# Kernel optimization log

Measured on AMD Instinct MI355X. Metric: run time of the kernel, lower is better.

## Reference

```python
import jax, jax.numpy as jnp
import numpy as np

N, C, V, L = 32, 32, 400, 64
GH_IN, GH = 64, [128, 64]
NUM_GRAPHS, ORDER, K, ALPHA = 2, 2, 20, 0.05
OUT_CH = 32
CAT_CH = C * (NUM_GRAPHS * ORDER + 1)
BN_EPS = 1e-5


def setup_inputs() -> dict:
    key = jax.random.key(0)
    ks = jax.random.split(key, 12)
    s = lambda fan_in: 1.0 / np.sqrt(fan_in)
    return {
        "inputs": jax.random.normal(ks[0], (N, C, V, L), jnp.float32),
        "adj_mats": jax.random.normal(ks[1], (V, V, GH_IN), jnp.float32),
        # edge MLP: Linear(64->128), ReLU, Linear(128->64), ReLU, Linear(64->num_graphs)
        "mlp_w0": jax.random.normal(ks[2], (GH_IN, GH[0]), jnp.float32) * s(GH_IN),
        "mlp_b0": jnp.zeros((GH[0],), jnp.float32),
        "mlp_w1": jax.random.normal(ks[3], (GH[0], GH[1]), jnp.float32) * s(GH[0]),
        "mlp_b1": jnp.zeros((GH[1],), jnp.float32),
        "mlp_w2": jax.random.normal(ks[4], (GH[1], NUM_GRAPHS), jnp.float32) * s(GH[1]),
        "mlp_b2": jnp.zeros((NUM_GRAPHS,), jnp.float32),
        # 1x1 Conv2d(in=160, out=32) == channel-mixing matmul
        "conv_w": jax.random.normal(ks[5], (OUT_CH, CAT_CH), jnp.float32) * s(CAT_CH),
        "conv_b": jnp.zeros((OUT_CH,), jnp.float32),
        "bn_gamma": jnp.ones((OUT_CH,), jnp.float32),
        "bn_beta": jnp.zeros((OUT_CH,), jnp.float32),
    }


def _sparsify(logits):
    # logits: [V, V]; softmax over rows, keep top-K per row, renormalize.
    adj = jax.nn.softmax(logits, axis=1)
    _, idx = jax.lax.top_k(adj, K)                     # [V, K]
    mask = jnp.zeros((V, V), adj.dtype).at[jnp.arange(V)[:, None], idx].set(1.0)
    adj = adj * mask
    return adj / (adj.sum(axis=1, keepdims=True) + 1e-8)


def reference(inputs, adj_mats, mlp_w0, mlp_b0, mlp_w1, mlp_b1, mlp_w2, mlp_b2,
              conv_w, conv_b, bn_gamma, bn_beta):
    # edge MLP on [V, V, GH_IN] -> [V, V, NUM_GRAPHS]
    h = jax.nn.relu(adj_mats @ mlp_w0 + mlp_b0)
    h = jax.nn.relu(h @ mlp_w1 + mlp_b1)
    g = h @ mlp_w2 + mlp_b2
    A = jax.vmap(_sparsify)(jnp.moveaxis(g, 2, 0))     # [NUM_GRAPHS, V, V]

    x = jax.nn.relu(inputs)                            # [N, C, V, L]
    outs = [x]
    for i in range(NUM_GRAPHS):
        y = x
        for _ in range(ORDER):
            y = ALPHA * x + (1.0 - ALPHA) * jnp.einsum('ncvl,vw->ncwl', y, A[i])
            outs.append(y)
    x1 = jnp.concatenate(outs, axis=1)                 # [N, CAT_CH, V, L]
    out = jnp.einsum('ncvl,oc->novl', x1, conv_w) + conv_b[None, :, None, None]

    # BatchNorm2d, training mode (batch statistics, biased variance)
    mean = out.mean(axis=(0, 2, 3), keepdims=True)
    var = out.var(axis=(0, 2, 3), keepdims=True)
    out = (out - mean) * jax.lax.rsqrt(var + BN_EPS)
    out = out * bn_gamma[None, :, None, None] + bn_beta[None, :, None, None]
    return out
```

## Files before the change

### kernel.cpp

```cpp
#include <hip/hip_runtime.h>


#define VDIM 400
#define VP   416
#define KV   (4*VP)
#define EROWS (5*VP)
#define OL   2048
#define ALPHA_ 0.05f
#define BETA_  0.95f

typedef short  bf16x8 __attribute__((ext_vector_type(8)));
typedef float  f32x4  __attribute__((ext_vector_type(4)));

__device__ inline unsigned short f2bf(float x){
  unsigned int u = __float_as_uint(x);
  unsigned int r = (u + 0x7fffu + ((u >> 16) & 1u)) >> 16;
  return (unsigned short)r;
}
__device__ inline float bf2f(unsigned short u){
  return __uint_as_float(((unsigned int)u) << 16);
}

__global__ __launch_bounds__(256) void k_mlp3(
    const float* __restrict__ adj,
    const float* __restrict__ w0, const float* __restrict__ b0,
    const float* __restrict__ w1, const float* __restrict__ b1,
    const float* __restrict__ w2, const float* __restrict__ b2,
    float* __restrict__ g)
{
  __shared__ __align__(16) float s_inT[64*68];
  __shared__ __align__(16) float s_h1 [64*72];
  __shared__ __align__(16) float s_red[4*64*2];
  const int tid  = threadIdx.x;
  const long ebase = (long)blockIdx.x * 64;
  const int wid  = __builtin_amdgcn_readfirstlane(tid >> 6);
  const int lane = tid & 63;

  #pragma unroll
  for (int i = 0; i < 4; ++i){
    const int idx = tid + i*256;
    const int row = idx >> 4, f4 = (idx & 15)*4;
    f32x4 v = *reinterpret_cast<const f32x4*>(&adj[(ebase + row)*64 + f4]);
    s_inT[(f4+0)*68 + row] = v.x;
    s_inT[(f4+1)*68 + row] = v.y;
    s_inT[(f4+2)*68 + row] = v.z;
    s_inT[(f4+3)*68 + row] = v.w;
  }
  __syncthreads();

  const int n0 = wid * 32;
  float h0[32];
  #pragma unroll
  for (int j = 0; j < 32; ++j) h0[j] = b0[n0 + j];
  #pragma unroll 2
  for (int f = 0; f < 64; ++f){
    const float a = s_inT[f*68 + lane];
    const float* __restrict__ wr = &w0[f*128 + n0];
    #pragma unroll
    for (int j = 0; j < 32; ++j) h0[j] = fmaf(a, wr[j], h0[j]);
  }
  #pragma unroll
  for (int j = 0; j < 32; ++j) h0[j] = fmaxf(h0[j], 0.f);

  float p[64];
  #pragma unroll
  for (int nh = 0; nh < 2; ++nh){
    float acc1[32];
    #pragma unroll
    for (int j = 0; j < 32; ++j) acc1[j] = 0.f;
    #pragma unroll 2
    for (int f = 0; f < 32; ++f){
      const float hv = h0[f];
      const float* __restrict__ wr = &w1[(n0 + f)*64 + nh*32];
      #pragma unroll
      for (int j = 0; j < 32; ++j) acc1[j] = fmaf(hv, wr[j], acc1[j]);
    }
    #pragma unroll
    for (int j = 0; j < 32; ++j) p[nh*32 + j] = acc1[j];
  }

  #pragma unroll
  for (int w = 0; w < 4; ++w){
    if (wid == w){
      if (w == 0){
        #pragma unroll
        for (int j = 0; j < 64; j += 4){
          f32x4 v = { p[j] + b1[j],   p[j+1] + b1[j+1],
                      p[j+2] + b1[j+2], p[j+3] + b1[j+3] };
          *reinterpret_cast<f32x4*>(&s_h1[lane*72 + j]) = v;
        }
      } else {
        #pragma unroll
        for (int j = 0; j < 64; j += 4){
          f32x4 v = *reinterpret_cast<f32x4*>(&s_h1[lane*72 + j]);
          v.x += p[j]; v.y += p[j+1]; v.z += p[j+2]; v.w += p[j+3];
          *reinterpret_cast<f32x4*>(&s_h1[lane*72 + j]) = v;
        }
      }
    }
    __syncthreads();
  }

  float q0 = 0.f, q1 = 0.f;
  #pragma unroll
  for (int j = 0; j < 16; ++j){
    const int n = wid*16 + j;
    const float hv = fmaxf(s_h1[lane*72 + n], 0.f);
    q0 = fmaf(hv, w2[n*2 + 0], q0);
    q1 = fmaf(hv, w2[n*2 + 1], q1);
  }
  s_red[(wid*64 + lane)*2 + 0] = q0;
  s_red[(wid*64 + lane)*2 + 1] = q1;
  __syncthreads();
  if (wid == 0){
    float r0 = b2[0], r1 = b2[1];
    #pragma unroll
    for (int w = 0; w < 4; ++w){
      r0 += s_red[(w*64 + lane)*2 + 0];
      r1 += s_red[(w*64 + lane)*2 + 1];
    }
    g[(ebase + lane)*2 + 0] = r0;
    g[(ebase + lane)*2 + 1] = r1;
  }
}

__global__ __launch_bounds__(256) void k_sparsify(
    const float* __restrict__ g, float* __restrict__ Bf)
{
  const int row = blockIdx.x, gr = blockIdx.y, tid = threadIdx.x;
  const int wid = tid >> 6, lane = tid & 63;
  __shared__ float s_v[4]; __shared__ int s_i[4];
  __shared__ float s_p[512];
  __shared__ int   s_sel[512];
  const int i0 = tid, i1 = tid + 256;
  float v0 = (i0 < VDIM) ? g[(row*VDIM + i0)*2 + gr] : -3.4e38f;
  float v1 = (i1 < VDIM) ? g[(row*VDIM + i1)*2 + gr] : -3.4e38f;

  float m = fmaxf(v0, v1);
  for (int off = 32; off > 0; off >>= 1) m = fmaxf(m, __shfl_down(m, off, 64));
  if (lane == 0) s_v[wid] = m;
  __syncthreads();
  const float rowmax = fmaxf(fmaxf(s_v[0], s_v[1]), fmaxf(s_v[2], s_v[3]));
  float p0 = (i0 < VDIM) ? expf(v0 - rowmax) : 0.f;
  float p1 = (i1 < VDIM) ? expf(v1 - rowmax) : 0.f;
  float zs = p0 + p1;
  for (int off = 32; off > 0; off >>= 1) zs += __shfl_down(zs, off, 64);
  __syncthreads();
  if (lane == 0) s_v[wid] = zs;
  __syncthreads();
  const float Z = s_v[0] + s_v[1] + s_v[2] + s_v[3];
  p0 /= Z; p1 /= Z;
  s_p[i0] = p0; s_p[i1] = p1;
  s_sel[i0] = (i0 < VDIM) ? 0 : 1;
  s_sel[i1] = (i1 < VDIM) ? 0 : 1;
  __syncthreads();

  float ssum = 0.f;
  for (int it = 0; it < 20; ++it){
    float cv = -1.f; int ci = 0x7fffffff;
    if (!s_sel[i0])              { cv = p0; ci = i0; }
    if (!s_sel[i1] && (p1 > cv)) { cv = p1; ci = i1; }
    for (int off = 32; off > 0; off >>= 1){
      float ov = __shfl_down(cv, off, 64); int oi = __shfl_down(ci, off, 64);
      if (ov > cv || (ov == cv && oi < ci)){ cv = ov; ci = oi; }
    }
    if (lane == 0){ s_v[wid] = cv; s_i[wid] = ci; }
    __syncthreads();
    float wv = s_v[0]; int wi_ = s_i[0];
    #pragma unroll
    for (int k = 1; k < 4; ++k){
      float ov = s_v[k]; int oi = s_i[k];
      if (ov > wv || (ov == wv && oi < wi_)){ wv = ov; wi_ = oi; }
    }
    ssum += wv;
    if (tid == (wi_ & 255)) s_sel[wi_] = 1;
    __syncthreads();
  }
  const float inv = 1.0f / (ssum + 1e-8f);
  float* B1 = Bf + (size_t)(gr*2) * (VDIM*VDIM);
  if (i0 < VDIM) B1[(size_t)i0*VDIM + row] = s_sel[i0] ? (s_p[i0]*inv) : 0.f;
  if (i1 < VDIM) B1[(size_t)i1*VDIM + row] = s_sel[i1] ? (s_p[i1]*inv) : 0.f;
}

__global__ __launch_bounds__(256) void k_sq(float* __restrict__ Bf)
{
  const int gr = blockIdx.z;
  const float* S = Bf + (size_t)(2*gr)   * (VDIM*VDIM);
  float*       D = Bf + (size_t)(2*gr+1) * (VDIM*VDIM);
  const int tx = threadIdx.x & 15, ty = threadIdx.x >> 4;
  const int w = blockIdx.x*16 + ty, v = blockIdx.y*16 + tx;
  __shared__ float As[16][17], Bs[16][17];
  float acc = 0.f;
  for (int u0 = 0; u0 < VDIM; u0 += 16){
    As[ty][tx] = S[(size_t)w*VDIM + u0 + tx];
    Bs[ty][tx] = S[(size_t)(u0+ty)*VDIM + v];
    __syncthreads();
    #pragma unroll
    for (int u = 0; u < 16; ++u) acc += As[ty][u] * Bs[u][tx];
    __syncthreads();
  }
  D[(size_t)w*VDIM + v] = acc;
}

__global__ __launch_bounds__(256) void k_pack(
    const float* __restrict__ Bf, const float* __restrict__ conv_w,
    unsigned short* __restrict__ Bcat, unsigned short* __restrict__ Mpp,
    float* __restrict__ bns)
{
  const int idx = blockIdx.x*256 + threadIdx.x;
  if (idx < 512*KV){
    const int w = idx / KV, col = idx % KV;
    const int k1 = col / VP, v = col % VP;
    float val = (w < VDIM && v < VDIM) ? Bf[(size_t)k1*(VDIM*VDIM) + (size_t)w*VDIM + v] : 0.f;
    Bcat[idx] = f2bf(val);
  }
  if (blockIdx.x == 0){
    const float a = ALPHA_, b = BETA_;
    for (int mIdx = threadIdx.x; mIdx < 160*32; mIdx += 256){
      const int rowm = mIdx >> 5, c = mIdx & 31;
      const int k = rowm / 32, o = rowm & 31;
      float W[5];
      #pragma unroll
      for (int j = 0; j < 5; ++j) W[j] = conv_w[o*160 + j*32 + c];
      float val;
      if      (k == 0) val = W[0] + a*(W[1]+W[2]+W[3]+W[4]);
      else if (k == 1) val = b*W[1] + a*b*W[2];
      else if (k == 2) val = b*b*W[2];
      else if (k == 3) val = b*W[3] + a*b*W[4];
      else             val = b*b*W[4];
      Mpp[rowm*32 + c] = f2bf(val);
    }
    if (threadIdx.x < 64) bns[threadIdx.x] = 0.f;
  }
}

__global__ __launch_bounds__(640) void k_e(
    const float* __restrict__ x, const unsigned short* __restrict__ Mpp,
    unsigned short* __restrict__ e, int n0)
{
  const int v0 = blockIdx.x * 2;
  const int n = n0 + blockIdx.y;
  const int tid = threadIdx.x;
  unsigned short* en = e + (size_t)blockIdx.y * EROWS * OL;
  if (v0 >= VDIM){
    for (int i = tid; i < 5*256*2; i += 640){
      const int row = i >> 8;
      const int k = row >> 1, vv = row & 1;
      const int off = (i & 255) * 8;
      *reinterpret_cast<uint4*>(&en[(size_t)(k*VP + v0 + vv)*OL + off]) = make_uint4(0,0,0,0);
    }
    return;
  }
  __shared__ __align__(16) unsigned short s_xT[64*32];
  __shared__ __align__(16) unsigned short s_out[10*16*64];
  const int wid = tid >> 6, lane = tid & 63;
  const int l15 = lane & 15, q = lane >> 4;
  bf16x8 afrag = *reinterpret_cast<const bf16x8*>(&Mpp[(wid*16 + l15)*32 + q*8]);
  const f32x4 zero = {0.f, 0.f, 0.f, 0.f};

  #pragma unroll
  for (int vv = 0; vv < 2; ++vv){
    const int v = v0 + vv;
    if (vv) __syncthreads();
    if (tid < 512){
      const int c = tid >> 4, l4 = (tid & 15) * 4;
      float4 xv = *reinterpret_cast<const float4*>(x + ((size_t)n*32 + c)*25600 + (size_t)v*64 + l4);
      s_xT[(l4+0)*32 + c] = f2bf(fmaxf(xv.x, 0.f));
      s_xT[(l4+1)*32 + c] = f2bf(fmaxf(xv.y, 0.f));
      s_xT[(l4+2)*32 + c] = f2bf(fmaxf(xv.z, 0.f));
      s_xT[(l4+3)*32 + c] = f2bf(fmaxf(xv.w, 0.f));
    }
    __syncthreads();
    f32x4 acc[4];
    #pragma unroll
    for (int lt = 0; lt < 4; ++lt){
      bf16x8 bfrag = *reinterpret_cast<const bf16x8*>(&s_xT[(lt*16 + l15)*32 + q*8]);
      acc[lt] = __builtin_amdgcn_mfma_f32_16x16x32_bf16(afrag, bfrag, zero, 0, 0, 0);
    }
    unsigned short* so = &s_out[wid*1024];
    #pragma unroll
    for (int lt = 0; lt < 4; ++lt)
      #pragma unroll
      for (int r = 0; r < 4; ++r)
        so[(q*4 + r)*64 + lt*16 + l15] = f2bf(acc[lt][r]);
    const int k = wid >> 1, o0 = (wid & 1) * 16;
    const size_t gbase = (size_t)(k*VP + v)*OL + (size_t)o0*64;
    uint4 d0 = *reinterpret_cast<uint4*>(&so[lane*16]);
    uint4 d1 = *reinterpret_cast<uint4*>(&so[lane*16 + 8]);
    *reinterpret_cast<uint4*>(&en[gbase + lane*16])     = d0;
    *reinterpret_cast<uint4*>(&en[gbase + lane*16 + 8]) = d1;
  }
}

__global__ __launch_bounds__(256) void k_prop(
    const unsigned short* __restrict__ Bcat, const unsigned short* __restrict__ e,
    const float* __restrict__ conv_b, float* __restrict__ out,
    float* __restrict__ bns, int n0)
{
  const int mt = blockIdx.x, nt = blockIdx.y, np = blockIdx.z;
  const int tid = threadIdx.x;
  const int wid = tid >> 6, lane = tid & 63;
  const int l15 = lane & 15, q = lane >> 4;
  const int ww = wid & 1, wh = wid >> 1;
  const unsigned short* en = e + (size_t)np * EROWS * OL;
  __shared__ __align__(16) unsigned short s_a[128*40];
  __shared__ __align__(16) unsigned short s_b[128*40];
  const f32x4 zero = {0.f, 0.f, 0.f, 0.f};
  f32x4 acc[4][4];
  #pragma unroll
  for (int mi = 0; mi < 4; ++mi)
    #pragma unroll
    for (int ni = 0; ni < 4; ++ni) acc[mi][ni] = zero;
  const int w_base = mt*128, ol0 = nt*128;

  const int r2 = tid >> 4;
  const int sg = tid & 15;
  const int kb = r2 >> 2;
  const int kin2 = (2*r2) & 7;

  for (int kk = 0; kk < KV; kk += 32){
    #pragma unroll
    for (int i = 0; i < 2; ++i){
      const int idx = tid + i*256;
      const int m = idx >> 2, seg = idx & 3;
      uint4 d = *reinterpret_cast<const uint4*>(&Bcat[(size_t)(w_base + m)*KV + kk + seg*8]);
      *reinterpret_cast<uint4*>(&s_a[m*40 + seg*8]) = d;
    }
    {
      union { uint4 u; unsigned short s[8]; } d0, d1;
      d0.u = *reinterpret_cast<const uint4*>(&en[(size_t)(VP + kk + 2*r2    )*OL + ol0 + sg*8]);
      d1.u = *reinterpret_cast<const uint4*>(&en[(size_t)(VP + kk + 2*r2 + 1)*OL + ol0 + sg*8]);
      #pragma unroll
      for (int t = 0; t < 8; ++t){
        const int nn = sg*8 + t;
        const int slot = kb ^ ((nn >> 3) & 3) ^ ((nn >> 5) & 3);
        const unsigned int val = (unsigned int)d0.s[t] | ((unsigned int)d1.s[t] << 16);
        *reinterpret_cast<unsigned int*>(&s_b[nn*40 + slot*8 + kin2]) = val;
      }
    }
    __syncthreads();
    bf16x8 af[4], bfr[4];
    #pragma unroll
    for (int mi = 0; mi < 4; ++mi){
      const int m = ww*64 + mi*16 + l15;
      af[mi] = *reinterpret_cast<const bf16x8*>(&s_a[m*40 + q*8]);
    }
    #pragma unroll
    for (int ni = 0; ni < 4; ++ni){
      const int nn = wh*64 + ni*16 + l15;
      const int sl = q ^ ((nn >> 3) & 3) ^ ((nn >> 5) & 3);
      bfr[ni] = *reinterpret_cast<const bf16x8*>(&s_b[nn*40 + sl*8]);
    }
    #pragma unroll
    for (int mi = 0; mi < 4; ++mi)
      #pragma unroll
      for (int ni = 0; ni < 4; ++ni)
        acc[mi][ni] = __builtin_amdgcn_mfma_f32_16x16x32_bf16(af[mi], bfr[ni], acc[mi][ni], 0, 0, 0);
    __syncthreads();
  }

  const int n_g = n0 + np;
  const int o = (ol0 >> 6) + wh;
  const float cb = conv_b[o];
  float bsum = 0.f, bsq = 0.f;
  #pragma unroll
  for (int mi = 0; mi < 4; ++mi){
    #pragma unroll
    for (int ni = 0; ni < 4; ++ni){
      const int nloc = wh*64 + ni*16 + l15;
      const int ol = ol0 + nloc;
      const int l = ol & 63;
      #pragma unroll
      for (int r = 0; r < 4; ++r){
        const int w = w_base + ww*64 + mi*16 + q*4 + r;
        if (w < VDIM){
          float val = acc[mi][ni][r] + bf2f(en[(size_t)w*OL + ol]) + cb;
          out[(((size_t)n_g*32 + o)*VDIM + w)*64 + l] = val;
          bsum += val; bsq += val*val;
        }
      }
    }
  }
  for (int off = 32; off > 0; off >>= 1){
    bsum += __shfl_down(bsum, off, 64);
    bsq  += __shfl_down(bsq,  off, 64);
  }
  if (lane == 0){
    atomicAdd(&bns[o], bsum);
    atomicAdd(&bns[32 + o], bsq);
  }
}

__global__ __launch_bounds__(256) void k_bnapply(
    float* __restrict__ out, const float* __restrict__ bns,
    const float* __restrict__ gamma, const float* __restrict__ beta, int total4)
{
  const int idx = blockIdx.x*256 + threadIdx.x;
  if (idx >= total4) return;
  const int o = (int)(((long)idx*4 / 25600) & 31);
  const float invM = 1.f / 819200.f;
  const float mean = bns[o] * invM;
  const float var  = bns[32+o] * invM - mean*mean;
  const float inv  = 1.0f / sqrtf(var + 1e-5f);
  const float sc = inv * gamma[o];
  const float sh = beta[o] - mean * sc;
  float4 v = reinterpret_cast<float4*>(out)[idx];
  v.x = v.x*sc + sh; v.y = v.y*sc + sh; v.z = v.z*sc + sh; v.w = v.w*sc + sh;
  reinterpret_cast<float4*>(out)[idx] = v;
}

extern "C" void kernel_launch(void* const* d_in, const int* in_sizes, int n_in,
                              void* d_out, int out_size, void* d_ws, size_t ws_size,
                              hipStream_t stream)
{
  const float* x      = (const float*)d_in[0];
  const float* adj    = (const float*)d_in[1];
  const float* w0     = (const float*)d_in[2];
  const float* b0     = (const float*)d_in[3];
  const float* w1     = (const float*)d_in[4];
  const float* b1     = (const float*)d_in[5];
  const float* w2     = (const float*)d_in[6];
  const float* b2     = (const float*)d_in[7];
  const float* conv_w = (const float*)d_in[8];
  const float* conv_b = (const float*)d_in[9];
  const float* gamma  = (const float*)d_in[10];
  const float* beta   = (const float*)d_in[11];
  float* out = (float*)d_out;

  char* ws = (char*)d_ws;
  size_t off = 0;
  auto alloc = [&](size_t bytes) -> void* {
    void* p = ws + off;
    off = (off + bytes + 255) & ~(size_t)255;
    return p;
  };
  float*          g_   = (float*)         alloc((size_t)VDIM*VDIM*2*4);
  float*          Bf   = (float*)         alloc((size_t)4*VDIM*VDIM*4);
  unsigned short* Bcat = (unsigned short*)alloc((size_t)512*KV*2);
  unsigned short* Mpp  = (unsigned short*)alloc((size_t)160*32*2);
  float*          bns  = (float*)         alloc((size_t)64*4);
  const size_t per_n = (size_t)EROWS * OL * 2;
  size_t avail = (ws_size > off) ? (ws_size - off) : 0;
  int NC = (int)(avail / per_n);
  if (NC > 32) NC = 32;
  if (NC < 1) NC = 1;
  while (32 % NC) NC--;
  unsigned short* ebuf = (unsigned short*)(ws + off);

  k_mlp3<<<2500, 256, 0, stream>>>(adj, w0, b0, w1, b1, w2, b2, g_);
  k_sparsify<<<dim3(VDIM, 2), 256, 0, stream>>>(g_, Bf);
  k_sq<<<dim3(25, 25, 2), 256, 0, stream>>>(Bf);
  k_pack<<<(512*KV + 255)/256, 256, 0, stream>>>(Bf, conv_w, Bcat, Mpp, bns);
  for (int n0 = 0; n0 < 32; n0 += NC){
    k_e<<<dim3(VP/2, NC), 640, 0, stream>>>(x, Mpp, ebuf, n0);
    k_prop<<<dim3(4, 16, NC), 256, 0, stream>>>(Bcat, ebuf, conv_b, out, bns, n0);
  }
  k_bnapply<<<(26214400/4 + 255)/256, 256, 0, stream>>>(out, bns, gamma, beta, 26214400/4);
}
```

Before: 702.0 us.

## Double-buffer LDS tiles in k_prop and remap workgroups across XCDs

The propagation GEMM kernel now prefetches the next K-slice from global memory into registers while MFMAs run on the current LDS buffer. It uses two LDS buffers so each iteration needs one barrier instead of two. It also flattens the 3D grid to 1D and permutes block indices so that consecutive logical tiles land on the same XCD, aiming for better L2 reuse of the shared Bcat and e tiles. The cost is doubled LDS use and more live registers, which may reduce occupancy.

```diff
diff --git a/kernel.cpp b/kernel.cpp
--- a/kernel.cpp
+++ b/kernel.cpp
@@ -297,14 +297,20 @@
     const float* __restrict__ conv_b, float* __restrict__ out,
     float* __restrict__ bns, int n0)
 {
-  const int mt = blockIdx.x, nt = blockIdx.y, np = blockIdx.z;
+  const int nb = gridDim.x;
+  int wg = blockIdx.x;
+  if ((nb & 7) == 0){
+    const int per = nb >> 3;
+    wg = (wg & 7) * per + (wg >> 3);
+  }
+  const int mt = wg & 3, nt = (wg >> 2) & 15, np = wg >> 6;
   const int tid = threadIdx.x;
   const int wid = tid >> 6, lane = tid & 63;
   const int l15 = lane & 15, q = lane >> 4;
   const int ww = wid & 1, wh = wid >> 1;
   const unsigned short* en = e + (size_t)np * EROWS * OL;
-  __shared__ __align__(16) unsigned short s_a[128*40];
-  __shared__ __align__(16) unsigned short s_b[128*40];
+  __shared__ __align__(16) unsigned short s_a[2][128*40];
+  __shared__ __align__(16) unsigned short s_b[2][128*40];
   const f32x4 zero = {0.f, 0.f, 0.f, 0.f};
   f32x4 acc[4][4];
   #pragma unroll
@@ -313,51 +319,69 @@
     for (int ni = 0; ni < 4; ++ni) acc[mi][ni] = zero;
   const int w_base = mt*128, ol0 = nt*128;
 
-  const int r2 = tid >> 4;
-  const int sg = tid & 15;
-  const int kb = r2 >> 2;
+  const int am = tid >> 2, aseg = tid & 3;
+  const int r2 = tid >> 4, sg = tid & 15;
+  const int kb = (r2 >> 2) & 3;
   const int kin2 = (2*r2) & 7;
 
+  uint4 aR0, aR1, bV0, bV1;
+
+  #define LOADG(kk_)                                                          \
+    aR0 = *reinterpret_cast<const uint4*>(&Bcat[(size_t)(w_base + am     )*KV + (kk_) + aseg*8]); \
+    aR1 = *reinterpret_cast<const uint4*>(&Bcat[(size_t)(w_base + am + 64)*KV + (kk_) + aseg*8]); \
+    bV0 = *reinterpret_cast<const uint4*>(&en[(size_t)(VP + (kk_) + 2*r2    )*OL + ol0 + sg*8]);  \
+    bV1 = *reinterpret_cast<const uint4*>(&en[(size_t)(VP + (kk_) + 2*r2 + 1)*OL + ol0 + sg*8]);
+
+  #define STORES(buf_)                                                        \
+    *reinterpret_cast<uint4*>(&s_a[buf_][(am     )*40 + aseg*8]) = aR0;       \
+    *reinterpret_cast<uint4*>(&s_a[buf_][(am + 64)*40 + aseg*8]) = aR1;       \
+    {                                                                         \
+      union { uint4 u; unsigned short s[8]; } d0_, d1_;                       \
+      d0_.u = bV0; d1_.u = bV1;                                               \
+      _Pragma("unroll")                                                       \
+      for (int t = 0; t < 8; ++t){                                            \
+        const int nn = sg*8 + t;                                              \
+        const int slot = kb ^ ((nn >> 3) & 3) ^ ((nn >> 5) & 3);              \
+        const unsigned int val = (unsigned int)d0_.s[t] | ((unsigned int)d1_.s[t] << 16); \
+        *reinterpret_cast<unsigned int*>(&s_b[buf_][nn*40 + slot*8 + kin2]) = val; \
+      }                                                                       \
+    }
+
+  LOADG(0);
+  STORES(0);
+  __syncthreads();
+  int cur = 0;
+
   for (int kk = 0; kk < KV; kk += 32){
-    #pragma unroll
-    for (int i = 0; i < 2; ++i){
-      const int idx = tid + i*256;
-      const int m = idx >> 2, seg = idx & 3;
-      uint4 d = *reinterpret_cast<const uint4*>(&Bcat[(size_t)(w_base + m)*KV + kk + seg*8]);
-      *reinterpret_cast<uint4*>(&s_a[m*40 + seg*8]) = d;
-    }
-    {
-      union { uint4 u; unsigned short s[8]; } d0, d1;
-      d0.u = *reinterpret_cast<const uint4*>(&en[(size_t)(VP + kk + 2*r2    )*OL + ol0 + sg*8]);
-      d1.u = *reinterpret_cast<const uint4*>(&en[(size_t)(VP + kk + 2*r2 + 1)*OL + ol0 + sg*8]);
-      #pragma unroll
-      for (int t = 0; t < 8; ++t){
-        const int nn = sg*8 + t;
-        const int slot = kb ^ ((nn >> 3) & 3) ^ ((nn >> 5) & 3);
-        const unsigned int val = (unsigned int)d0.s[t] | ((unsigned int)d1.s[t] << 16);
-        *reinterpret_cast<unsigned int*>(&s_b[nn*40 + slot*8 + kin2]) = val;
-      }
-    }
-    __syncthreads();
+    const bool more = (kk + 32 < KV);
+    if (more){ LOADG(kk + 32); }
+
     bf16x8 af[4], bfr[4];
     #pragma unroll
     for (int mi = 0; mi < 4; ++mi){
       const int m = ww*64 + mi*16 + l15;
-      af[mi] = *reinterpret_cast<const bf16x8*>(&s_a[m*40 + q*8]);
+      af[mi] = *reinterpret_cast<const bf16x8*>(&s_a[cur][m*40 + q*8]);
     }
     #pragma unroll
     for (int ni = 0; ni < 4; ++ni){
       const int nn = wh*64 + ni*16 + l15;
       const int sl = q ^ ((nn >> 3) & 3) ^ ((nn >> 5) & 3);
-      bfr[ni] = *reinterpret_cast<const bf16x8*>(&s_b[nn*40 + sl*8]);
+      bfr[ni] = *reinterpret_cast<const bf16x8*>(&s_b[cur][nn*40 + sl*8]);
     }
     #pragma unroll
     for (int mi = 0; mi < 4; ++mi)
       #pragma unroll
       for (int ni = 0; ni < 4; ++ni)
         acc[mi][ni] = __builtin_amdgcn_mfma_f32_16x16x32_bf16(af[mi], bfr[ni], acc[mi][ni], 0, 0, 0);
-    __syncthreads();
-  }
+
+    if (more){
+      STORES(cur ^ 1);
+      __syncthreads();
+    }
+    cur ^= 1;
+  }
+  #undef LOADG
+  #undef STORES
 
   const int n_g = n0 + np;
   const int o = (ol0 >> 6) + wh;
@@ -453,7 +477,7 @@
   k_pack<<<(512*KV + 255)/256, 256, 0, stream>>>(Bf, conv_w, Bcat, Mpp, bns);
   for (int n0 = 0; n0 < 32; n0 += NC){
     k_e<<<dim3(VP/2, NC), 640, 0, stream>>>(x, Mpp, ebuf, n0);
-    k_prop<<<dim3(4, 16, NC), 256, 0, stream>>>(Bcat, ebuf, conv_b, out, bns, n0);
+    k_prop<<<4*16*NC, 256, 0, stream>>>(Bcat, ebuf, conv_b, out, bns, n0);
   }
   k_bnapply<<<(26214400/4 + 255)/256, 256, 0, stream>>>(out, bns, gamma, beta, 26214400/4);
 }
```

After: 725.9 us. +3.4%, slower.
